# Optimization experiments

Hardware: AMD Instinct MI355X
Metric: run time of the kernel (lower is better)

## Reference

```python
import jax, jax.numpy as jnp
import numpy as np
from jax import lax


def setup_inputs() -> dict:
    key = jax.random.key(0)
    kx, kw = jax.random.split(key)
    X = jax.random.normal(kx, (16, 64, 224, 224), dtype=jnp.float32)
    W = jax.random.normal(kw, (1, 1, 3, 3), dtype=jnp.float32)
    return {"X": X, "W": W}


def reference(X, W):
    # Original: ZeroPad2d(1), then slide a single (k,k) filter over every
    # channel independently (filter broadcasts over B and C; sum over k,k).
    # This is a depthwise conv where every channel shares the SAME kernel.
    B, C, H, Wd = X.shape
    Xp = jnp.pad(X, ((0, 0), (0, 0), (1, 1), (1, 1)))  # ZeroPad2d(1)
    kern = jnp.tile(W, (C, 1, 1, 1))  # (C, 1, k, k) — shared weights per channel
    out = lax.conv_general_dilated(
        Xp, kern,
        window_strides=(1, 1),
        padding='VALID',
        dimension_numbers=('NCHW', 'OIHW', 'NCHW'),
        feature_group_count=C,
    )
    return out  # [B, C, 224, 224]
```

## Files before the change

kernel.cpp:

```cpp
#include <hip/hip_runtime.h>


#define HH 224
#define WW 224
#define X4T 56
#define STRIPS 8
#define SH 28

typedef float f4 __attribute__((ext_vector_type(4)));

__device__ __forceinline__ void load_row6(float r[6], const float* rp,
                                          bool yok, bool xl, bool xr) {
    if (yok) {
        f4 v = *(const f4*)rp;
        r[0] = xl ? rp[-1] : 0.f;
        r[1] = v.x; r[2] = v.y; r[3] = v.z; r[4] = v.w;
        r[5] = xr ? rp[4] : 0.f;
    } else {
        r[0] = r[1] = r[2] = r[3] = r[4] = r[5] = 0.f;
    }
}

__global__ __launch_bounds__(256) void dwconv3x3_strip(
    const float* __restrict__ X, const float* __restrict__ Wk,
    float* __restrict__ Out, int nThreads)
{
    int idx = blockIdx.x * 256 + threadIdx.x;
    if (idx >= nThreads) return;

    int x4    = idx % X4T;
    int t     = idx / X4T;
    int strip = t % STRIPS;
    int p     = t / STRIPS;

    const float w00 = Wk[0], w01 = Wk[1], w02 = Wk[2];
    const float w10 = Wk[3], w11 = Wk[4], w12 = Wk[5];
    const float w20 = Wk[6], w21 = Wk[7], w22 = Wk[8];

    const int  x0 = x4 * 4;
    const int  y0 = strip * SH;
    const bool xl = (x0 > 0);
    const bool xr = (x0 + 4 < WW);

    const float* plane  = X   + (size_t)p * (HH * WW) + x0;
    float*       oplane = Out + (size_t)p * (HH * WW) + x0;

    float a[6], b[6], c[6];
    load_row6(a, plane + (y0 - 1) * WW, y0 > 0, xl, xr);
    load_row6(b, plane + (y0    ) * WW, true,   xl, xr);

    #pragma unroll 4
    for (int j = 0; j < SH; ++j) {
        const int yn = y0 + j + 1;
        load_row6(c, plane + yn * WW, yn < HH, xl, xr);

        f4 o;
        #pragma unroll
        for (int ci = 0; ci < 4; ++ci) {
            float acc;
            acc  = w00 * a[ci] + w01 * a[ci + 1] + w02 * a[ci + 2];
            acc += w10 * b[ci] + w11 * b[ci + 1] + w12 * b[ci + 2];
            acc += w20 * c[ci] + w21 * c[ci + 1] + w22 * c[ci + 2];
            o[ci] = acc;
        }
        __builtin_nontemporal_store(o, (f4*)(oplane + (y0 + j) * WW));

        #pragma unroll
        for (int q = 0; q < 6; ++q) { a[q] = b[q]; b[q] = c[q]; }
    }
}

extern "C" void kernel_launch(void* const* d_in, const int* in_sizes, int n_in,
                              void* d_out, int out_size, void* d_ws, size_t ws_size,
                              hipStream_t stream) {
    const float* X  = (const float*)d_in[0];
    const float* Wk = (const float*)d_in[1];
    float* Out = (float*)d_out;

    const int nPlanes  = 16 * 64;
    const int nThreads = nPlanes * STRIPS * X4T;
    const int threads  = 256;
    const int blocks   = (nThreads + threads - 1) / threads;

    dwconv3x3_strip<<<blocks, threads, 0, stream>>>(X, Wk, Out, nThreads);
}
```

Before: 356.8 us.

## Use short 8-row tiles with all loads issued upfront and XCD-aware block remap

Each thread now computes an 8x4 output tile instead of a 28-row strip, so there are more threads and each one loads all ten input rows up front before computing, which raises memory-level parallelism. Block IDs are permuted so consecutive logical workgroups land on the same XCD, aiming for better L2 locality of the halo rows. The cost is more halo re-reads (10 rows loaded per 8 rows output instead of 30 per 28) and higher register use. The bounds check is dropped because the thread count divides evenly by 256, and the remap assumes the grid size is a multiple of 8.

```diff
diff --git a/kernel.cpp b/kernel.cpp
--- a/kernel.cpp
+++ b/kernel.cpp
@@ -4,69 +4,67 @@
 #define HH 224
 #define WW 224
 #define X4T 56
-#define STRIPS 8
-#define SH 28
+#define YT  28
+#define TH  8
 
 typedef float f4 __attribute__((ext_vector_type(4)));
 
-__device__ __forceinline__ void load_row6(float r[6], const float* rp,
-                                          bool yok, bool xl, bool xr) {
-    if (yok) {
-        f4 v = *(const f4*)rp;
-        r[0] = xl ? rp[-1] : 0.f;
-        r[1] = v.x; r[2] = v.y; r[3] = v.z; r[4] = v.w;
-        r[5] = xr ? rp[4] : 0.f;
-    } else {
-        r[0] = r[1] = r[2] = r[3] = r[4] = r[5] = 0.f;
-    }
-}
+__global__ __launch_bounds__(256) void dwconv3x3_8x4(
+    const float* __restrict__ X, const float* __restrict__ Wk,
+    float* __restrict__ Out)
+{
+    const int nwg = gridDim.x;
+    const int cpx = nwg >> 3;
+    const int b   = blockIdx.x;
+    const int wg  = (b & 7) * cpx + (b >> 3);
 
-__global__ __launch_bounds__(256) void dwconv3x3_strip(
-    const float* __restrict__ X, const float* __restrict__ Wk,
-    float* __restrict__ Out, int nThreads)
-{
-    int idx = blockIdx.x * 256 + threadIdx.x;
-    if (idx >= nThreads) return;
+    const int idx = wg * 256 + (int)threadIdx.x;
 
-    int x4    = idx % X4T;
-    int t     = idx / X4T;
-    int strip = t % STRIPS;
-    int p     = t / STRIPS;
+    const int x4 = idx % X4T;
+    const int t  = idx / X4T;
+    const int ys = t % YT;
+    const int p  = t / YT;
 
     const float w00 = Wk[0], w01 = Wk[1], w02 = Wk[2];
     const float w10 = Wk[3], w11 = Wk[4], w12 = Wk[5];
     const float w20 = Wk[6], w21 = Wk[7], w22 = Wk[8];
 
     const int  x0 = x4 * 4;
-    const int  y0 = strip * SH;
+    const int  y0 = ys * TH;
     const bool xl = (x0 > 0);
     const bool xr = (x0 + 4 < WW);
 
     const float* plane  = X   + (size_t)p * (HH * WW) + x0;
     float*       oplane = Out + (size_t)p * (HH * WW) + x0;
 
-    float a[6], b[6], c[6];
-    load_row6(a, plane + (y0 - 1) * WW, y0 > 0, xl, xr);
-    load_row6(b, plane + (y0    ) * WW, true,   xl, xr);
+    float r[TH + 2][6];
+    #pragma unroll
+    for (int q = 0; q < TH + 2; ++q) {
+        const int  yr  = y0 - 1 + q;
+        const bool yok = (yr >= 0) && (yr < HH);
+        const float* rp = plane + yr * WW;
+        if (yok) {
+            f4 v = *(const f4*)rp;
+            r[q][0] = xl ? rp[-1] : 0.f;
+            r[q][1] = v.x; r[q][2] = v.y; r[q][3] = v.z; r[q][4] = v.w;
+            r[q][5] = xr ? rp[4] : 0.f;
+        } else {
+            r[q][0] = r[q][1] = r[q][2] = r[q][3] = r[q][4] = r[q][5] = 0.f;
+        }
+    }
 
-    #pragma unroll 4
-    for (int j = 0; j < SH; ++j) {
-        const int yn = y0 + j + 1;
-        load_row6(c, plane + yn * WW, yn < HH, xl, xr);
-
+    #pragma unroll
+    for (int j = 0; j < TH; ++j) {
         f4 o;
         #pragma unroll
         for (int ci = 0; ci < 4; ++ci) {
             float acc;
-            acc  = w00 * a[ci] + w01 * a[ci + 1] + w02 * a[ci + 2];
-            acc += w10 * b[ci] + w11 * b[ci + 1] + w12 * b[ci + 2];
-            acc += w20 * c[ci] + w21 * c[ci + 1] + w22 * c[ci + 2];
+            acc  = w00 * r[j+0][ci] + w01 * r[j+0][ci+1] + w02 * r[j+0][ci+2];
+            acc += w10 * r[j+1][ci] + w11 * r[j+1][ci+1] + w12 * r[j+1][ci+2];
+            acc += w20 * r[j+2][ci] + w21 * r[j+2][ci+1] + w22 * r[j+2][ci+2];
             o[ci] = acc;
         }
         __builtin_nontemporal_store(o, (f4*)(oplane + (y0 + j) * WW));
-
-        #pragma unroll
-        for (int q = 0; q < 6; ++q) { a[q] = b[q]; b[q] = c[q]; }
     }
 }
 
@@ -78,9 +76,9 @@
     float* Out = (float*)d_out;
 
     const int nPlanes  = 16 * 64;
-    const int nThreads = nPlanes * STRIPS * X4T;
+    const int nThreads = nPlanes * YT * X4T;
     const int threads  = 256;
-    const int blocks   = (nThreads + threads - 1) / threads;
+    const int blocks   = nThreads / threads;
 
-    dwconv3x3_strip<<<blocks, threads, 0, stream>>>(X, Wk, Out, nThreads);
+    dwconv3x3_8x4<<<blocks, threads, 0, stream>>>(X, Wk, Out);
 }
```

Result: faster. 349.0 us (-2.2%).
